# Kernel optimization log

Measured on AMD Instinct MI355X. Metric: run time of the kernel, lower is better.

The kernel has to match this reference:

```python
import jax, jax.numpy as jnp
import numpy as np

NUM_HEADS = 8
BN_EPS = 1e-3  # keras BatchNormalization default epsilon


def setup_inputs() -> dict:
    key = jax.random.key(0)
    ks = jax.random.split(key, 4)
    B, N, C, s, H = 8, 1024, 3, 16, NUM_HEADS
    dim = s * s * C  # 768
    return {
        "x": jax.random.normal(ks[0], (B, N, dim), jnp.float32),
        "qconv_w": jax.random.normal(ks[1], (3, 3, C, C), jnp.float32) * 0.1,  # HWIO, shared q/k/v (source bug, faithful)
        "reatten_w": jax.random.normal(ks[2], (H, H), jnp.float32) * 0.2,      # 1x1 conv mixing heads
        "reatten_b": jnp.zeros((H,), jnp.float32),
        "bn_gamma": jnp.ones((H,), jnp.float32),
        "bn_beta": jnp.zeros((H,), jnp.float32),
        "bn_mean": jnp.zeros((H,), jnp.float32),
        "bn_var": jnp.ones((H,), jnp.float32),
        "proj_w": jax.random.normal(ks[3], (dim, dim), jnp.float32) * 0.02,
        "proj_b": jnp.zeros((dim,), jnp.float32),
    }


def reference(x, qconv_w, reatten_w, reatten_b, bn_gamma, bn_beta, bn_mean, bn_var, proj_w, proj_b):
    H = NUM_HEADS
    B, N, P = x.shape
    C = qconv_w.shape[2]
    s = int(np.sqrt(P // C))
    hd = P // H
    scale = hd ** -0.5

    # unflatten: tokens become conv batch; 3x3 same conv, no bias
    xim = x.reshape(B * N, s, s, C)
    y = jax.lax.conv_general_dilated(
        xim, qconv_w, window_strides=(1, 1), padding='SAME',
        dimension_numbers=('NHWC', 'HWIO', 'NHWC'))
    # source applies qconv2d for q, k AND v -> identical projections
    q = y.reshape(B, N, H, hd).transpose(0, 2, 1, 3)  # [B,H,N,hd]

    attn = jax.nn.softmax(jnp.einsum('bhnd,bhmd->bhnm', q, q) * scale, axis=-1)

    # re-attention: 1x1 conv across heads + inference batchnorm (per head channel), reatten_scale=1.0
    re = jnp.einsum('bhnm,hg->bgnm', attn, reatten_w) + reatten_b[None, :, None, None]
    st = lambda a: a[None, :, None, None]
    attn_next = (re - st(bn_mean)) * st(bn_gamma) / jnp.sqrt(st(bn_var) + BN_EPS) + st(bn_beta)

    out = jnp.einsum('bgnm,bgmd->bngd', attn_next, q).reshape(B, N, P)
    xo = out @ proj_w + proj_b
    return (xo, attn_next)
```

## Files before the change

kernel.cpp:

```cpp
#include <hip/hip_runtime.h>

#define NB 8
#define NN 1024
#define NH 8
#define HD 96
#define DIM 768

typedef __bf16 bf16x8 __attribute__((ext_vector_type(8)));
typedef float f32x4 __attribute__((ext_vector_type(4)));
typedef unsigned short u16x8 __attribute__((ext_vector_type(8)));

__device__ __forceinline__ ushort f2bf(float f) {
  uint u = __float_as_uint(f);
  u += 0x7fffu + ((u >> 16) & 1u);
  return (ushort)(u >> 16);
}
__device__ __forceinline__ float bf2f(ushort u) {
  return __uint_as_float(((uint)u) << 16);
}

__global__ __launch_bounds__(256) void k_prep_w(const float* __restrict__ pw,
                                                ushort* __restrict__ wT) {
  __shared__ ushort tile[64][72];
  int d0 = blockIdx.x * 64;
  int j0 = blockIdx.y * 64;
  int t = threadIdx.x;
  {
    int r = t >> 2;
    int ch = (t & 3) * 16;
    const float* src = pw + (size_t)(d0 + r) * DIM + j0 + ch;
#pragma unroll
    for (int i = 0; i < 16; i += 4) {
      float4 v = *(const float4*)(src + i);
      tile[ch + i + 0][r] = f2bf(v.x);
      tile[ch + i + 1][r] = f2bf(v.y);
      tile[ch + i + 2][r] = f2bf(v.z);
      tile[ch + i + 3][r] = f2bf(v.w);
    }
  }
  __syncthreads();
  {
    int j = t >> 2;
    int ch = (t & 3) * 16;
    union { ushort u[16]; uint4 v[2]; } tmp;
#pragma unroll
    for (int i = 0; i < 16; ++i) tmp.u[i] = tile[j][ch + i];
    uint4* dst = (uint4*)(wT + (size_t)(j0 + j) * DIM + d0 + ch);
    dst[0] = tmp.v[0]; dst[1] = tmp.v[1];
  }
}

__global__ __launch_bounds__(256) void k_conv(const float* __restrict__ x,
                                              const float* __restrict__ w,
                                              ushort* __restrict__ q) {
  __shared__ float xs[768];
  __shared__ float ws[81];
  __shared__ ushort os[768];
  int token = blockIdx.x;
  int t = threadIdx.x;
  const float4* xin = (const float4*)(x + (size_t)token * DIM);
  if (t < 192) ((float4*)xs)[t] = xin[t];
  if (t < 81) ws[t] = w[t];
  __syncthreads();
  int r = t >> 4, c = t & 15;
  float a0 = 0.f, a1 = 0.f, a2 = 0.f;
#pragma unroll
  for (int dr = 0; dr < 3; ++dr) {
    int rr = r + dr - 1;
    bool rok = (rr >= 0) & (rr < 16);
#pragma unroll
    for (int dc = 0; dc < 3; ++dc) {
      int cc = c + dc - 1;
      bool ok = rok & (cc >= 0) & (cc < 16);
#pragma unroll
      for (int ci = 0; ci < 3; ++ci) {
        int idx = ok ? (rr * 16 + cc) * 3 + ci : 0;
        float xv = xs[idx];
        xv = ok ? xv : 0.f;
        const float* wp = ws + ((dr * 3 + dc) * 3 + ci) * 3;
        a0 += xv * wp[0]; a1 += xv * wp[1]; a2 += xv * wp[2];
      }
    }
  }
  os[t * 3 + 0] = f2bf(a0);
  os[t * 3 + 1] = f2bf(a1);
  os[t * 3 + 2] = f2bf(a2);
  __syncthreads();
  uint4* dst = (uint4*)(q + (size_t)token * DIM);
  if (t < 96) dst[t] = ((const uint4*)os)[t];
}

__global__ __launch_bounds__(256) void k_transpose_q(const ushort* __restrict__ q,
                                                     ushort* __restrict__ qT) {
  __shared__ ushort tile[64][72];
  int bb = blockIdx.z;
  int n0 = blockIdx.x * 64;
  int d0 = blockIdx.y * 64;
  int t = threadIdx.x;
  {
    int r = t >> 2;
    int cq = (t & 3) * 16;
    const ushort* src = q + ((size_t)(bb * NN) + n0 + r) * DIM + d0 + cq;
    uint4 v0 = *(const uint4*)src;
    uint4 v1 = *(const uint4*)(src + 8);
    *(uint4*)&tile[r][cq] = v0;
    *(uint4*)&tile[r][cq + 8] = v1;
  }
  __syncthreads();
  {
    int d = t >> 2;
    int nch = (t & 3) * 16;
    union { ushort u[16]; uint4 v[2]; } tmp;
#pragma unroll
    for (int j = 0; j < 16; ++j) tmp.u[j] = tile[nch + j][d];
    uint4* dst = (uint4*)(qT + ((size_t)(bb * DIM) + d0 + d) * NN + n0 + nch);
    dst[0] = tmp.v[0]; dst[1] = tmp.v[1];
  }
}

__global__ __launch_bounds__(128) void k_colsum(const ushort* __restrict__ q,
                                                float* __restrict__ cs) {
  int bb = blockIdx.y;
  int c = blockIdx.x * 128 + threadIdx.x;
  const ushort* p = q + (size_t)bb * NN * DIM + c;
  float s = 0.f;
#pragma unroll 16
  for (int n = 0; n < NN; ++n) s += bf2f(p[(size_t)n * DIM]);
  cs[bb * DIM + c] = s;
}

__global__ __launch_bounds__(512, 2) void k_attn_fused(
    const ushort* __restrict__ q, const ushort* __restrict__ qT,
    const float* __restrict__ cs,
    const float* __restrict__ rw, const float* __restrict__ rb,
    const float* __restrict__ gamma, const float* __restrict__ beta,
    const float* __restrict__ mean, const float* __restrict__ var,
    float* __restrict__ attn, ushort* __restrict__ outb) {
  __shared__ ushort P[16384];

  const int lin = blockIdx.x;
  const int bb = lin & 7;
  const int nt = lin >> 3;
  const int n0 = nt * 32;
  const int t = threadIdx.x;
  const int w = t >> 6, lane = t & 63;
  const int lm = lane & 15, lg = lane >> 4;
  const float scale = 0.10206207261596575f;

  float wreg[8];
#pragma unroll
  for (int h = 0; h < 8; ++h) wreg[h] = rw[h * 8 + w];
  const float effs = gamma[w] * __frsqrt_rn(var[w] + 1e-3f);
  const float effb = (rb[w] - mean[w]) * effs + beta[w];

  const ushort* qb = q + (size_t)bb * NN * DIM;
  const ushort* vb = qT + (size_t)bb * DIM * NN;

  bf16x8 qf[2][3];
#pragma unroll
  for (int nf = 0; nf < 2; ++nf)
#pragma unroll
    for (int ks = 0; ks < 3; ++ks)
      qf[nf][ks] = *(const bf16x8*)(qb + (size_t)(n0 + nf * 16 + lm) * DIM
                                     + w * HD + ks * 32 + lg * 8);

  float rs[2][4];
#pragma unroll
  for (int nf = 0; nf < 2; ++nf)
#pragma unroll
    for (int r = 0; r < 4; ++r) rs[nf][r] = 0.f;

  for (int mt = 0; mt < 16; ++mt) {
    const int m0 = mt * 64;
    f32x4 sacc[2][4] = {};
#pragma unroll
    for (int ks = 0; ks < 3; ++ks) {
      bf16x8 kf[4];
#pragma unroll
      for (int mf = 0; mf < 4; ++mf)
        kf[mf] = *(const bf16x8*)(qb + (size_t)(m0 + mf * 16 + lm) * DIM
                                   + w * HD + ks * 32 + lg * 8);
#pragma unroll
      for (int nf = 0; nf < 2; ++nf)
#pragma unroll
        for (int mf = 0; mf < 4; ++mf)
          sacc[nf][mf] = __builtin_amdgcn_mfma_f32_16x16x32_bf16(qf[nf][ks], kf[mf], sacc[nf][mf], 0, 0, 0);
    }
#pragma unroll
    for (int nf = 0; nf < 2; ++nf)
#pragma unroll
      for (int mf = 0; mf < 4; ++mf)
#pragma unroll
        for (int r = 0; r < 4; ++r)
          rs[nf][r] += __expf(sacc[nf][mf][r] * scale);
  }
  float inv[2][4];
#pragma unroll
  for (int nf = 0; nf < 2; ++nf)
#pragma unroll
    for (int r = 0; r < 4; ++r) {
      float s = rs[nf][r];
      s += __shfl_xor(s, 1); s += __shfl_xor(s, 2);
      s += __shfl_xor(s, 4); s += __shfl_xor(s, 8);
      inv[nf][r] = 1.f / s;
    }

  f32x4 oacc[2][6] = {};

  for (int mt = 0; mt < 16; ++mt) {
    const int m0 = mt * 64;
    {
      f32x4 sacc[2][4] = {};
#pragma unroll
      for (int ks = 0; ks < 3; ++ks) {
        bf16x8 kf[4];
#pragma unroll
        for (int mf = 0; mf < 4; ++mf)
          kf[mf] = *(const bf16x8*)(qb + (size_t)(m0 + mf * 16 + lm) * DIM
                                     + w * HD + ks * 32 + lg * 8);
#pragma unroll
        for (int nf = 0; nf < 2; ++nf)
#pragma unroll
          for (int mf = 0; mf < 4; ++mf)
            sacc[nf][mf] = __builtin_amdgcn_mfma_f32_16x16x32_bf16(qf[nf][ks], kf[mf], sacc[nf][mf], 0, 0, 0);
      }
#pragma unroll
      for (int nf = 0; nf < 2; ++nf)
#pragma unroll
        for (int mf = 0; mf < 4; ++mf)
#pragma unroll
          for (int r = 0; r < 4; ++r) {
            float e = __expf(sacc[nf][mf][r] * scale) * inv[nf][r];
            int n = nf * 16 + lg * 4 + r;
            int mbyte = 2 * (mf * 16 + lm);
            int addr = w * 4096 + n * 128 + (mbyte ^ ((n & 7) << 4));
            *(ushort*)((char*)P + addr) = f2bf(e);
          }
    }
    bf16x8 vf[2][6];
#pragma unroll
    for (int ks = 0; ks < 2; ++ks)
#pragma unroll
      for (int df = 0; df < 6; ++df)
        vf[ks][df] = *(const bf16x8*)(vb + (size_t)(w * HD + df * 16 + lm) * NN
                                       + m0 + ks * 32 + lg * 8);
    __syncthreads();
    bf16x8 pmf[2][2];
#pragma unroll
    for (int nf = 0; nf < 2; ++nf) {
      int n = nf * 16 + lm;
      int swz = (n & 7) << 4;
#pragma unroll
      for (int ks = 0; ks < 2; ++ks) {
        int rbase = n * 128 + ((2 * (ks * 32 + lg * 8)) ^ swz);
        float mix[8];
#pragma unroll
        for (int j = 0; j < 8; ++j) mix[j] = 0.f;
#pragma unroll
        for (int h = 0; h < 8; ++h) {
          u16x8 pu = *(const u16x8*)((char*)P + h * 4096 + rbase);
#pragma unroll
          for (int j = 0; j < 8; ++j) mix[j] += bf2f(pu[j]) * wreg[h];
        }
        f32x4 o0, o1;
        o0[0] = mix[0] * effs + effb; o0[1] = mix[1] * effs + effb;
        o0[2] = mix[2] * effs + effb; o0[3] = mix[3] * effs + effb;
        o1[0] = mix[4] * effs + effb; o1[1] = mix[5] * effs + effb;
        o1[2] = mix[6] * effs + effb; o1[3] = mix[7] * effs + effb;
        size_t arow = ((size_t)(bb * 8 + w) * NN + (n0 + n)) * NN + m0 + ks * 32 + lg * 8;
        __builtin_nontemporal_store(o0, (f32x4*)(attn + arow));
        __builtin_nontemporal_store(o1, (f32x4*)(attn + arow + 4));
        u16x8 pk;
#pragma unroll
        for (int j = 0; j < 8; ++j) pk[j] = f2bf(mix[j]);
        pmf[nf][ks] = *(bf16x8*)&pk;
      }
    }
    __syncthreads();
#pragma unroll
    for (int ks = 0; ks < 2; ++ks)
#pragma unroll
      for (int df = 0; df < 6; ++df)
#pragma unroll
        for (int nf = 0; nf < 2; ++nf)
          oacc[nf][df] = __builtin_amdgcn_mfma_f32_16x16x32_bf16(pmf[nf][ks], vf[ks][df], oacc[nf][df], 0, 0, 0);
  }

#pragma unroll
  for (int df = 0; df < 6; ++df) {
    int col = w * HD + df * 16 + lm;
    float csv = cs[bb * DIM + col] * effb;
#pragma unroll
    for (int nf = 0; nf < 2; ++nf)
#pragma unroll
      for (int r = 0; r < 4; ++r) {
        int row = n0 + nf * 16 + lg * 4 + r;
        outb[(size_t)(bb * NN + row) * DIM + col] =
            f2bf(oacc[nf][df][r] * effs + csv);
      }
  }
}

__global__ __launch_bounds__(256) void k_proj(const ushort* __restrict__ outb,
                                              const ushort* __restrict__ wT,
                                              const float* __restrict__ pb,
                                              float* __restrict__ xo) {
  __shared__ ushort As[128][72];
  __shared__ ushort Bs[128][72];
  int m0 = blockIdx.x * 128;
  int j0 = blockIdx.y * 128;
  int t = threadIdx.x;
  int wv = t >> 6, lane = t & 63;
  int wr = (wv >> 1) * 64, wc = (wv & 1) * 64;
  int lm = lane & 15, lg = lane >> 4;
  f32x4 acc[4][4] = {};
  for (int kk = 0; kk < 12; ++kk) {
    int k0 = kk * 64;
    __syncthreads();
    for (int i = t; i < 1024; i += 256) {
      int row = i >> 3;
      int c = (i & 7) * 8;
      *(uint4*)&As[row][c] = *(const uint4*)(outb + (size_t)(m0 + row) * DIM + k0 + c);
      *(uint4*)&Bs[row][c] = *(const uint4*)(wT + (size_t)(j0 + row) * DIM + k0 + c);
    }
    __syncthreads();
#pragma unroll
    for (int ks = 0; ks < 2; ++ks) {
      bf16x8 af[4], bfr[4];
#pragma unroll
      for (int mi = 0; mi < 4; ++mi)
        af[mi] = *(const bf16x8*)&As[wr + mi * 16 + lm][ks * 32 + lg * 8];
#pragma unroll
      for (int ni = 0; ni < 4; ++ni)
        bfr[ni] = *(const bf16x8*)&Bs[wc + ni * 16 + lm][ks * 32 + lg * 8];
#pragma unroll
      for (int mi = 0; mi < 4; ++mi)
#pragma unroll
        for (int ni = 0; ni < 4; ++ni)
          acc[mi][ni] = __builtin_amdgcn_mfma_f32_16x16x32_bf16(af[mi], bfr[ni], acc[mi][ni], 0, 0, 0);
    }
  }
#pragma unroll
  for (int ni = 0; ni < 4; ++ni) {
    int col = j0 + wc + ni * 16 + lm;
    float bias = pb[col];
#pragma unroll
    for (int mi = 0; mi < 4; ++mi)
#pragma unroll
      for (int r = 0; r < 4; ++r) {
        int row = m0 + wr + mi * 16 + lg * 4 + r;
        xo[(size_t)row * DIM + col] = acc[mi][ni][r] + bias;
      }
  }
}

extern "C" void kernel_launch(void* const* d_in, const int* in_sizes, int n_in,
                              void* d_out, int out_size, void* d_ws, size_t ws_size,
                              hipStream_t stream) {
  (void)in_sizes; (void)n_in; (void)out_size; (void)ws_size;
  const float* x       = (const float*)d_in[0];
  const float* qconv_w = (const float*)d_in[1];
  const float* rw      = (const float*)d_in[2];
  const float* rb      = (const float*)d_in[3];
  const float* gamma   = (const float*)d_in[4];
  const float* beta    = (const float*)d_in[5];
  const float* mean    = (const float*)d_in[6];
  const float* var     = (const float*)d_in[7];
  const float* pw      = (const float*)d_in[8];
  const float* pb      = (const float*)d_in[9];

  float* xo   = (float*)d_out;
  float* attn = xo + (size_t)NB * NN * DIM;

  char* ws = (char*)d_ws;
  ushort* q    = (ushort*)(ws);
  ushort* qT   = (ushort*)(ws + 12582912);
  ushort* wT   = (ushort*)(ws + 25165824);
  ushort* outb = (ushort*)(ws + 26345472);
  float*  csum = (float*)(ws + 38928384);

  hipLaunchKernelGGL(k_prep_w, dim3(12, 12), dim3(256), 0, stream, pw, wT);
  hipLaunchKernelGGL(k_conv, dim3(NB * NN), dim3(256), 0, stream, x, qconv_w, q);
  hipLaunchKernelGGL(k_transpose_q, dim3(16, 12, NB), dim3(256), 0, stream, q, qT);
  hipLaunchKernelGGL(k_colsum, dim3(6, NB), dim3(128), 0, stream, q, csum);
  hipLaunchKernelGGL(k_attn_fused, dim3(256), dim3(512), 0, stream, q, qT, csum,
                     rw, rb, gamma, beta, mean, var, attn, outb);
  hipLaunchKernelGGL(k_proj, dim3(64, 6), dim3(256), 0, stream, outb, wT, pb, xo);
}
```

Before: 290.6 us.

## Halve attention row tile, double-buffer P in LDS, raise occupancy

The fused attention kernel now handles 16 query rows per block instead of 32, which doubles the grid to 512 blocks and lets launch bounds ask for 4 blocks per CU. The shared P buffer is split into two halves that alternate by tile, so one barrier per iteration replaces two. K fragments for all k-steps are loaded before the MFMAs. This aims to fill the MI355X's CUs better and cut sync stalls. In exchange, K and V are re-read from global memory twice as often per query row, and the softmax sum pass is recomputed per block.

New measurement: 569.6 us. 1.96x slower.

```diff
diff --git a/kernel.cpp b/kernel.cpp
--- a/kernel.cpp
+++ b/kernel.cpp
@@ -129,19 +129,19 @@
   cs[bb * DIM + c] = s;
 }
 
-__global__ __launch_bounds__(512, 2) void k_attn_fused(
+__global__ __launch_bounds__(512, 4) void k_attn_fused(
     const ushort* __restrict__ q, const ushort* __restrict__ qT,
     const float* __restrict__ cs,
     const float* __restrict__ rw, const float* __restrict__ rb,
     const float* __restrict__ gamma, const float* __restrict__ beta,
     const float* __restrict__ mean, const float* __restrict__ var,
     float* __restrict__ attn, ushort* __restrict__ outb) {
-  __shared__ ushort P[16384];
+  __shared__ ushort P[2][8192];
 
   const int lin = blockIdx.x;
   const int bb = lin & 7;
   const int nt = lin >> 3;
-  const int n0 = nt * 32;
+  const int n0 = nt * 16;
   const int t = threadIdx.x;
   const int w = t >> 6, lane = t & 63;
   const int lm = lane & 15, lg = lane >> 4;
@@ -156,87 +156,73 @@
   const ushort* qb = q + (size_t)bb * NN * DIM;
   const ushort* vb = qT + (size_t)bb * DIM * NN;
 
-  bf16x8 qf[2][3];
-#pragma unroll
-  for (int nf = 0; nf < 2; ++nf)
-#pragma unroll
-    for (int ks = 0; ks < 3; ++ks)
-      qf[nf][ks] = *(const bf16x8*)(qb + (size_t)(n0 + nf * 16 + lm) * DIM
-                                     + w * HD + ks * 32 + lg * 8);
-
-  float rs[2][4];
-#pragma unroll
-  for (int nf = 0; nf < 2; ++nf)
-#pragma unroll
-    for (int r = 0; r < 4; ++r) rs[nf][r] = 0.f;
-
+  bf16x8 qf[3];
+#pragma unroll
+  for (int ks = 0; ks < 3; ++ks)
+    qf[ks] = *(const bf16x8*)(qb + (size_t)(n0 + lm) * DIM + w * HD + ks * 32 + lg * 8);
+
+  float rs[4] = {0.f, 0.f, 0.f, 0.f};
   for (int mt = 0; mt < 16; ++mt) {
     const int m0 = mt * 64;
-    f32x4 sacc[2][4] = {};
-#pragma unroll
-    for (int ks = 0; ks < 3; ++ks) {
-      bf16x8 kf[4];
+    bf16x8 kf[3][4];
+#pragma unroll
+    for (int ks = 0; ks < 3; ++ks)
 #pragma unroll
       for (int mf = 0; mf < 4; ++mf)
-        kf[mf] = *(const bf16x8*)(qb + (size_t)(m0 + mf * 16 + lm) * DIM
-                                   + w * HD + ks * 32 + lg * 8);
-#pragma unroll
-      for (int nf = 0; nf < 2; ++nf)
-#pragma unroll
-        for (int mf = 0; mf < 4; ++mf)
-          sacc[nf][mf] = __builtin_amdgcn_mfma_f32_16x16x32_bf16(qf[nf][ks], kf[mf], sacc[nf][mf], 0, 0, 0);
-    }
-#pragma unroll
-    for (int nf = 0; nf < 2; ++nf)
+        kf[ks][mf] = *(const bf16x8*)(qb + (size_t)(m0 + mf * 16 + lm) * DIM
+                                       + w * HD + ks * 32 + lg * 8);
+    f32x4 sacc[4] = {};
+#pragma unroll
+    for (int ks = 0; ks < 3; ++ks)
 #pragma unroll
       for (int mf = 0; mf < 4; ++mf)
-#pragma unroll
-        for (int r = 0; r < 4; ++r)
-          rs[nf][r] += __expf(sacc[nf][mf][r] * scale);
-  }
-  float inv[2][4];
-#pragma unroll
-  for (int nf = 0; nf < 2; ++nf)
-#pragma unroll
-    for (int r = 0; r < 4; ++r) {
-      float s = rs[nf][r];
-      s += __shfl_xor(s, 1); s += __shfl_xor(s, 2);
-      s += __shfl_xor(s, 4); s += __shfl_xor(s, 8);
-      inv[nf][r] = 1.f / s;
-    }
-
-  f32x4 oacc[2][6] = {};
+        sacc[mf] = __builtin_amdgcn_mfma_f32_16x16x32_bf16(qf[ks], kf[ks][mf], sacc[mf], 0, 0, 0);
+#pragma unroll
+    for (int mf = 0; mf < 4; ++mf)
+#pragma unroll
+      for (int r = 0; r < 4; ++r)
+        rs[r] += __expf(sacc[mf][r] * scale);
+  }
+  float inv[4];
+#pragma unroll
+  for (int r = 0; r < 4; ++r) {
+    float s = rs[r];
+    s += __shfl_xor(s, 1); s += __shfl_xor(s, 2);
+    s += __shfl_xor(s, 4); s += __shfl_xor(s, 8);
+    inv[r] = 1.f / s;
+  }
+
+  f32x4 oacc[6] = {};
 
   for (int mt = 0; mt < 16; ++mt) {
     const int m0 = mt * 64;
+    char* Pc = (char*)P + (mt & 1) * 16384;
     {
-      f32x4 sacc[2][4] = {};
-#pragma unroll
-      for (int ks = 0; ks < 3; ++ks) {
-        bf16x8 kf[4];
+      bf16x8 kf[3][4];
+#pragma unroll
+      for (int ks = 0; ks < 3; ++ks)
 #pragma unroll
         for (int mf = 0; mf < 4; ++mf)
-          kf[mf] = *(const bf16x8*)(qb + (size_t)(m0 + mf * 16 + lm) * DIM
-                                     + w * HD + ks * 32 + lg * 8);
-#pragma unroll
-        for (int nf = 0; nf < 2; ++nf)
-#pragma unroll
-          for (int mf = 0; mf < 4; ++mf)
-            sacc[nf][mf] = __builtin_amdgcn_mfma_f32_16x16x32_bf16(qf[nf][ks], kf[mf], sacc[nf][mf], 0, 0, 0);
-      }
-#pragma unroll
-      for (int nf = 0; nf < 2; ++nf)
+          kf[ks][mf] = *(const bf16x8*)(qb + (size_t)(m0 + mf * 16 + lm) * DIM
+                                         + w * HD + ks * 32 + lg * 8);
+      f32x4 sacc[4] = {};
+#pragma unroll
+      for (int ks = 0; ks < 3; ++ks)
 #pragma unroll
         for (int mf = 0; mf < 4; ++mf)
-#pragma unroll
-          for (int r = 0; r < 4; ++r) {
-            float e = __expf(sacc[nf][mf][r] * scale) * inv[nf][r];
-            int n = nf * 16 + lg * 4 + r;
-            int mbyte = 2 * (mf * 16 + lm);
-            int addr = w * 4096 + n * 128 + (mbyte ^ ((n & 7) << 4));
-            *(ushort*)((char*)P + addr) = f2bf(e);
-          }
-    }
+          sacc[mf] = __builtin_amdgcn_mfma_f32_16x16x32_bf16(qf[ks], kf[ks][mf], sacc[mf], 0, 0, 0);
+#pragma unroll
+      for (int mf = 0; mf < 4; ++mf)
+#pragma unroll
+        for (int r = 0; r < 4; ++r) {
+          float e = __expf(sacc[mf][r] * scale) * inv[r];
+          int n = lg * 4 + r;
+          int mbyte = 2 * (mf * 16 + lm);
+          int addr = w * 2048 + n * 128 + (mbyte ^ ((n & 7) << 4));
+          *(ushort*)(Pc + addr) = f2bf(e);
+        }
+    }
+    __syncthreads();
     bf16x8 vf[2][6];
 #pragma unroll
     for (int ks = 0; ks < 2; ++ks)
@@ -244,11 +230,9 @@
       for (int df = 0; df < 6; ++df)
         vf[ks][df] = *(const bf16x8*)(vb + (size_t)(w * HD + df * 16 + lm) * NN
                                        + m0 + ks * 32 + lg * 8);
-    __syncthreads();
-    bf16x8 pmf[2][2];
-#pragma unroll
-    for (int nf = 0; nf < 2; ++nf) {
-      int n = nf * 16 + lm;
+    bf16x8 pmf[2];
+    {
+      int n = lm;
       int swz = (n & 7) << 4;
 #pragma unroll
       for (int ks = 0; ks < 2; ++ks) {
@@ -258,7 +242,7 @@
         for (int j = 0; j < 8; ++j) mix[j] = 0.f;
 #pragma unroll
         for (int h = 0; h < 8; ++h) {
-          u16x8 pu = *(const u16x8*)((char*)P + h * 4096 + rbase);
+          u16x8 pu = *(const u16x8*)(Pc + h * 2048 + rbase);
 #pragma unroll
           for (int j = 0; j < 8; ++j) mix[j] += bf2f(pu[j]) * wreg[h];
         }
@@ -273,17 +257,14 @@
         u16x8 pk;
 #pragma unroll
         for (int j = 0; j < 8; ++j) pk[j] = f2bf(mix[j]);
-        pmf[nf][ks] = *(bf16x8*)&pk;
+        pmf[ks] = *(bf16x8*)&pk;
       }
     }
-    __syncthreads();
 #pragma unroll
     for (int ks = 0; ks < 2; ++ks)
 #pragma unroll
       for (int df = 0; df < 6; ++df)
-#pragma unroll
-        for (int nf = 0; nf < 2; ++nf)
-          oacc[nf][df] = __builtin_amdgcn_mfma_f32_16x16x32_bf16(pmf[nf][ks], vf[ks][df], oacc[nf][df], 0, 0, 0);
+        oacc[df] = __builtin_amdgcn_mfma_f32_16x16x32_bf16(pmf[ks], vf[ks][df], oacc[df], 0, 0, 0);
   }
 
 #pragma unroll
@@ -291,13 +272,10 @@
     int col = w * HD + df * 16 + lm;
     float csv = cs[bb * DIM + col] * effb;
 #pragma unroll
-    for (int nf = 0; nf < 2; ++nf)
-#pragma unroll
-      for (int r = 0; r < 4; ++r) {
-        int row = n0 + nf * 16 + lg * 4 + r;
-        outb[(size_t)(bb * NN + row) * DIM + col] =
-            f2bf(oacc[nf][df][r] * effs + csv);
-      }
+    for (int r = 0; r < 4; ++r) {
+      int row = n0 + lg * 4 + r;
+      outb[(size_t)(bb * NN + row) * DIM + col] = f2bf(oacc[df][r] * effs + csv);
+    }
   }
 }
 
@@ -383,7 +361,7 @@
   hipLaunchKernelGGL(k_conv, dim3(NB * NN), dim3(256), 0, stream, x, qconv_w, q);
   hipLaunchKernelGGL(k_transpose_q, dim3(16, 12, NB), dim3(256), 0, stream, q, qT);
   hipLaunchKernelGGL(k_colsum, dim3(6, NB), dim3(128), 0, stream, q, csum);
-  hipLaunchKernelGGL(k_attn_fused, dim3(256), dim3(512), 0, stream, q, qT, csum,
+  hipLaunchKernelGGL(k_attn_fused, dim3(512), dim3(512), 0, stream, q, qT, csum,
                      rw, rb, gamma, beta, mean, var, attn, outb);
   hipLaunchKernelGGL(k_proj, dim3(64, 6), dim3(256), 0, stream, outb, wT, pb, xo);
 }
```
